# Performance work log

Measured on AMD Instinct MI355X. Metric: run time of the kernel, lower is better.

The kernel has to match this reference:

```python
import jax, jax.numpy as jnp
import numpy as np

N_QUBITS = 4  # matches init n_qubits; depth = 1


def _apply_rx(state, angles, wire):
    # state: (B, 2**N) complex64; angles: (B,) real. RX(theta) = [[c, -is],[-is, c]], c=cos(t/2), s=sin(t/2)
    B = state.shape[0]
    left = 2 ** wire
    st = state.reshape(B, left, 2, -1)
    half = angles * 0.5
    c = jnp.cos(half).astype(jnp.complex64).reshape(B, 1, 1)
    s = ((-1j) * jnp.sin(half).astype(jnp.complex64)).reshape(B, 1, 1)
    s0 = st[:, :, 0, :]
    s1 = st[:, :, 1, :]
    out = jnp.stack([c * s0 + s * s1, s * s0 + c * s1], axis=2)
    return out.reshape(B, -1)


def _apply_cnot(state, ctrl):
    # CNOT on wires [ctrl, ctrl+1]: flip target amplitudes where control bit is 1
    B = state.shape[0]
    left = 2 ** ctrl
    st = state.reshape(B, left, 2, 2, -1)
    st = st.at[:, :, 1, :, :].set(st[:, :, 1, ::-1, :])
    return st.reshape(B, -1)


def _qgate(angles, theta):
    # angles: (B, N_QUBITS) data-encoded RX angles; theta: (N_QUBITS,) trainable RX angles
    # Circuit: RX(data) on each wire -> CNOT chain -> RX(theta) on each wire -> <Z_i> per wire
    B = angles.shape[0]
    state = jnp.zeros((B, 2 ** N_QUBITS), jnp.complex64).at[:, 0].set(1.0 + 0.0j)
    for i in range(N_QUBITS):
        state = _apply_rx(state, angles[:, i], i)
    for i in range(N_QUBITS - 1):
        state = _apply_cnot(state, i)
    for i in range(N_QUBITS):
        state = _apply_rx(state, jnp.broadcast_to(theta[i], (B,)), i)
    probs = jnp.real(state * jnp.conj(state)).reshape((B,) + (2,) * N_QUBITS)
    expz = []
    for i in range(N_QUBITS):
        axes = tuple(a for a in range(1, N_QUBITS + 1) if a != i + 1)
        p = probs.sum(axis=axes)  # (B, 2)
        expz.append(p[:, 0] - p[:, 1])
    return jnp.stack(expz, axis=1)  # (B, N_QUBITS)


def setup_inputs() -> dict:
    key = jax.random.key(0)
    ks = jax.random.split(key, 16)
    T, B, D, H, Q = 256, 512, 128, 128, N_QUBITS

    def w(k, shape, scale=0.05):
        return jax.random.normal(k, shape, jnp.float32) * scale

    inp = {
        'inputs': jax.random.normal(ks[0], (T, B, D), jnp.float32),
        'hx0': jnp.zeros((B, H), jnp.float32),
        'cx0': jnp.zeros((B, H), jnp.float32),
    }
    for j, n in enumerate(['f', 'i', 'g', 'o']):
        inp['W' + n] = w(ks[1 + j], (H, D + H))
        inp['b' + n] = jnp.zeros((H,), jnp.float32)
        inp['W' + n + 'q'] = w(ks[5 + j], (Q, D + H))
        inp['b' + n + 'q'] = jnp.zeros((Q,), jnp.float32)
        inp['th' + n] = jax.random.normal(ks[9 + j], (Q,), jnp.float32)
    inp['Wq'] = w(ks[13], (H, Q))
    inp['bq'] = jnp.zeros((H,), jnp.float32)
    return inp


def reference(inputs, hx0, cx0, Wf, bf, Wfq, bfq, thf, Wi, bi, Wiq, biq, thi,
              Wg, bg, Wgq, bgq, thg, Wo, bo, Woq, boq, tho, Wq, bq):
    def step(carry, x):
        hx, cx = carry
        comb = jnp.concatenate([x, hx], axis=1)  # (B, D+H)

        def lin(W, b):
            return comb @ W.T + b

        def qg(Wl, bl, th):
            return _qgate(lin(Wl, bl), th) @ Wq.T + bq

        f = jax.nn.sigmoid(lin(Wf, bf)) + jax.nn.sigmoid(qg(Wfq, bfq, thf))
        i = jax.nn.sigmoid(lin(Wi, bi)) + jax.nn.sigmoid(qg(Wiq, biq, thi))
        g = jnp.tanh(lin(Wg, bg)) + jnp.tanh(qg(Wgq, bgq, thg))
        o = jax.nn.sigmoid(lin(Wo, bo)) + jax.nn.sigmoid(qg(Woq, boq, tho))
        cx2 = f * cx + i * g
        hx2 = o * jnp.tanh(cx2)
        return (hx2, cx2), hx2

    (hxT, cxT), outs = jax.lax.scan(step, (hx0, cx0), inputs)
    return outs, (hxT, cxT)
```

## Files before the change

### kernel.cpp

```cpp
#include <hip/hip_runtime.h>
#include <cmath>

#define TT 256
#define BB 512
#define DD 128
#define HH 128
#define NCOL 528
#define KK 256
#define NCPAD 576

__global__ __launch_bounds__(256) void pack_weights(
    const float* __restrict__ Wf, const float* __restrict__ bf,
    const float* __restrict__ Wfq, const float* __restrict__ bfq,
    const float* __restrict__ Wi, const float* __restrict__ bi,
    const float* __restrict__ Wiq, const float* __restrict__ biq,
    const float* __restrict__ Wg, const float* __restrict__ bg,
    const float* __restrict__ Wgq, const float* __restrict__ bgq,
    const float* __restrict__ Wo, const float* __restrict__ bo,
    const float* __restrict__ Woq, const float* __restrict__ boq,
    float* __restrict__ Wxp, float* __restrict__ Whr3,
    float* __restrict__ Whql, float* __restrict__ bcat)
{
    int idx = blockIdx.x * blockDim.x + threadIdx.x;
    if (idx < NCOL * KK) {
        int c = idx >> 8, k = idx & 255;
        const float* srcW; int cl;
        if (c < 512) { int g = c >> 7; cl = c & 127;
            srcW = (g == 0) ? Wf : (g == 1) ? Wi : (g == 2) ? Wg : Wo; }
        else { int g = (c - 512) >> 2; cl = (c - 512) & 3;
            srcW = (g == 0) ? Wfq : (g == 1) ? Wiq : (g == 2) ? Wgq : Woq; }
        float v = srcW[(size_t)cl * KK + k];
        if (k < 128) Wxp[(size_t)c * 128 + k] = v;
        else {
            int kk = k - 128;
            if (c < 512) {
                int gate = c >> 7, hcol = c & 127;
                int t = hcol * 4 + (kk >> 5);
                int j = gate * 8 + ((kk >> 2) & 7);
                Whr3[((size_t)j * 512 + t) * 4 + (kk & 3)] = v;
            } else {
                Whql[(size_t)(c - 512) * 128 + kk] = v;
            }
        }
    }
    if (idx < NCPAD) {
        float b = 0.f;
        int c = idx;
        if (c < 512) { int g = c >> 7; int cl = c & 127;
            b = (g == 0) ? bf[cl] : (g == 1) ? bi[cl] : (g == 2) ? bg[cl] : bo[cl]; }
        else if (c < NCOL) { int g = (c - 512) >> 2; int cl = (c - 512) & 3;
            b = (g == 0) ? bfq[cl] : (g == 1) ? biq[cl] : (g == 2) ? bgq[cl] : boq[cl]; }
        bcat[c] = b;
    }
}

#define P1_BM 128
#define P1_BN 64
#define ATP 132
#define BTP 68
__global__ __launch_bounds__(256, 3) void xgemm(
    const float* __restrict__ X, const float* __restrict__ Wxp,
    const float* __restrict__ bcat, float* __restrict__ Zx)
{
    __shared__ float At[64][ATP];
    __shared__ float Bt[64][BTP];
    const int tid = threadIdx.x;
    const int m0 = blockIdx.x * P1_BM;
    const int c0 = blockIdx.y * P1_BN;
    const int tm = tid >> 3;
    const int tn = tid & 7;
    float acc[4][8] = {};

    for (int khf = 0; khf < 2; ++khf) {
        #pragma unroll
        for (int j = 0; j < 8; ++j) {
            int fidx = tid + 256 * j;
            int m = fidx >> 4, k4 = (fidx & 15) * 4;
            float4 v = *(const float4*)(X + (size_t)(m0 + m) * 128 + khf * 64 + k4);
            At[k4 + 0][m] = v.x; At[k4 + 1][m] = v.y; At[k4 + 2][m] = v.z; At[k4 + 3][m] = v.w;
        }
        #pragma unroll
        for (int j = 0; j < 4; ++j) {
            int fidx = tid + 256 * j;
            int c = fidx >> 4, k4 = (fidx & 15) * 4;
            int cg = c0 + c;
            float4 v = make_float4(0.f, 0.f, 0.f, 0.f);
            if (cg < NCOL) v = *(const float4*)(Wxp + (size_t)cg * 128 + khf * 64 + k4);
            Bt[k4 + 0][c] = v.x; Bt[k4 + 1][c] = v.y; Bt[k4 + 2][c] = v.z; Bt[k4 + 3][c] = v.w;
        }
        __syncthreads();
        #pragma unroll 4
        for (int k = 0; k < 64; ++k) {
            float4 a  = *(const float4*)&At[k][tm * 4];
            float4 b0 = *(const float4*)&Bt[k][tn * 8];
            float4 b1 = *(const float4*)&Bt[k][tn * 8 + 4];
            float av[4] = {a.x, a.y, a.z, a.w};
            float bv[8] = {b0.x, b0.y, b0.z, b0.w, b1.x, b1.y, b1.z, b1.w};
            #pragma unroll
            for (int i = 0; i < 4; ++i)
                #pragma unroll
                for (int j = 0; j < 8; ++j)
                    acc[i][j] = fmaf(av[i], bv[j], acc[i][j]);
        }
        __syncthreads();
    }
    int c = c0 + tn * 8;
    if (c < NCOL) {
        float4 ba = *(const float4*)(bcat + c);
        float4 bb = *(const float4*)(bcat + c + 4);
        #pragma unroll
        for (int i = 0; i < 4; ++i) {
            int m = m0 + tm * 4 + i;
            float4 o0, o1;
            o0.x = acc[i][0] + ba.x; o0.y = acc[i][1] + ba.y;
            o0.z = acc[i][2] + ba.z; o0.w = acc[i][3] + ba.w;
            o1.x = acc[i][4] + bb.x; o1.y = acc[i][5] + bb.y;
            o1.z = acc[i][6] + bb.z; o1.w = acc[i][7] + bb.w;
            *(float4*)(Zx + (size_t)m * NCOL + c)     = o0;
            *(float4*)(Zx + (size_t)m * NCOL + c + 4) = o1;
        }
    }
}

__device__ __forceinline__ float sigm(float x) { return 1.0f / (1.0f + __expf(-x)); }
__device__ __forceinline__ float tanh_f(float x) {
    float e = __expf(2.f * x);
    return 1.f - 2.f / (e + 1.f);
}

#define FMA4(acc, Wv, Xv) acc = fmaf((Wv).x, (Xv).x, fmaf((Wv).y, (Xv).y, fmaf((Wv).z, (Xv).z, fmaf((Wv).w, (Xv).w, (acc)))))
#define PIN4(Wv) asm volatile("" : "+v"((Wv).x), "+v"((Wv).y), "+v"((Wv).z), "+v"((Wv).w))

#define DPPRED(v) { \
    v += __int_as_float(__builtin_amdgcn_update_dpp(0, __float_as_int(v), 0xB1, 0xF, 0xF, true)); \
    v += __int_as_float(__builtin_amdgcn_update_dpp(0, __float_as_int(v), 0x4E, 0xF, 0xF, true)); }

__device__ __forceinline__ int hsk(int k) { return k + 8 * (k >> 5); }

__global__ __launch_bounds__(512)
__attribute__((amdgpu_waves_per_eu(2, 2)))
void qlstm_rec(
    const float* __restrict__ Zx,
    const float* __restrict__ Whr3,
    const float* __restrict__ Whql,
    const float* __restrict__ hx0, const float* __restrict__ cx0,
    float* __restrict__ stateH, float* __restrict__ stateC,
    const float* __restrict__ Wq, const float* __restrict__ bq,
    const float* __restrict__ thf, const float* __restrict__ thi,
    const float* __restrict__ thg, const float* __restrict__ tho,
    float* __restrict__ out, int t0, int TC)
{
    __shared__ __align__(16) float hL[2][152];
    __shared__ __align__(16) float cEd[2][20];
    __shared__ __align__(16) float cEc[2][20];

    const int tid  = threadIdx.x;
    const int row0 = blockIdx.x * 2;
    const int ks   = tid & 3;
    const int h    = tid >> 2;

    const float4* Wp3 = (const float4*)Whr3;
    float4 wv[32];
    #pragma unroll
    for (int j = 0; j < 32; ++j) wv[j] = Wp3[j * 512 + tid];
    #pragma unroll
    for (int j = 0; j < 32; ++j) PIN4(wv[j]);

    const bool isCell = (ks < 2);
    const int  r      = ks & 1;
    float4 wqv = make_float4(0.f, 0.f, 0.f, 0.f);
    float bb = 0.f, cxr = 0.f;
    if (isCell) {
        wqv = *(const float4*)(Wq + h * 4);
        bb  = bq[h];
    }
    const bool isQ = (tid & 15) < 4;
    const int qi = tid >> 4;
    const int rq = qi & 1, qc = qi >> 1;
    const int qg = qc >> 2, qw = qc & 3;
    float qcoef = 1.f, qth3 = 0.f;
    float4 qw4[8] = {};
    if (isQ) {
        const float* thp = (qg == 0) ? thf : (qg == 1) ? thi : (qg == 2) ? thg : tho;
        qcoef = (qw < 3) ? cosf(thp[qw]) : 1.f;
        qth3  = thp[3];
        const float4* qp = (const float4*)(Whql + (size_t)qc * 128 + ks * 32);
        #pragma unroll
        for (int j = 0; j < 8; ++j) qw4[j] = qp[j];
    }
    if (isCell) {
        const float* hs = (t0 == 0) ? hx0 : stateH;
        const float* cs = (t0 == 0) ? cx0 : stateC;
        hL[r][hsk(h)] = hs[(size_t)(row0 + r) * HH + h];
        cxr           = cs[(size_t)(row0 + r) * HH + h];
    }
    __syncthreads();

    for (int tc = 0; tc < TC; ++tc) {
        const float* zrow = Zx + ((size_t)tc * BB + row0) * NCOL;
        float zc0 = 0, zc1 = 0, zc2 = 0, zc3 = 0, zqv = 0;
        if (isCell) {
            const float* zp = zrow + (size_t)r * NCOL + h;
            zc0 = zp[0]; zc1 = zp[128]; zc2 = zp[256]; zc3 = zp[384];
        }
        if (isQ) zqv = zrow[(size_t)rq * NCOL + 512 + qc];

        float aF0 = 0, aF1 = 0, aI0 = 0, aI1 = 0, aG0 = 0, aG1 = 0, aO0 = 0, aO1 = 0;
        float qa = 0.f;
        {
            const float4* h0p = (const float4*)&hL[0][40 * ks];
            const float4* h1p = (const float4*)&hL[1][40 * ks];
            #pragma unroll
            for (int k4 = 0; k4 < 8; ++k4) {
                float4 hv0 = h0p[k4];
                float4 hv1 = h1p[k4];
                FMA4(aF0, wv[k4],      hv0);  FMA4(aF1, wv[k4],      hv1);
                FMA4(aI0, wv[8 + k4],  hv0);  FMA4(aI1, wv[8 + k4],  hv1);
                FMA4(aG0, wv[16 + k4], hv0);  FMA4(aG1, wv[16 + k4], hv1);
                FMA4(aO0, wv[24 + k4], hv0);  FMA4(aO1, wv[24 + k4], hv1);
                float4 hq;
                hq.x = rq ? hv1.x : hv0.x; hq.y = rq ? hv1.y : hv0.y;
                hq.z = rq ? hv1.z : hv0.z; hq.w = rq ? hv1.w : hv0.w;
                FMA4(qa, qw4[k4], hq);
            }
        }
        DPPRED(aF0) DPPRED(aF1) DPPRED(aI0) DPPRED(aI1)
        DPPRED(aG0) DPPRED(aG1) DPPRED(aO0) DPPRED(aO1)
        DPPRED(qa)

        if (isQ) {
            float a = zqv + qa;
            float c = __cosf(a);
            float dval = (qw < 3) ? qcoef * c : __cosf(a + qth3);
            if (ks == 0) {
                cEd[rq][qc] = dval;
                cEc[rq][qc] = c;
            }
        }
        __syncthreads();

        if (isCell) {
            float pf = zc0 + (r ? aF1 : aF0);
            float pi = zc1 + (r ? aI1 : aI0);
            float pg = zc2 + (r ? aG1 : aG0);
            float po = zc3 + (r ? aO1 : aO0);
            float qz[4];
            #pragma unroll
            for (int g = 0; g < 4; ++g) {
                float4 dv = *(const float4*)&cEd[r][g * 4];
                float4 cv = *(const float4*)&cEc[r][g * 4];
                float c01  = cv.x * cv.y;
                float c012 = c01 * cv.z;
                qz[g] = fmaf(dv.x, wqv.x,
                        fmaf(dv.y * cv.x, wqv.y,
                        fmaf(dv.z * c01, wqv.z,
                        fmaf(dv.w * c012, wqv.w, bb))));
            }
            float f  = sigm(pf)   + sigm(qz[0]);
            float ii = sigm(pi)   + sigm(qz[1]);
            float gg = tanh_f(pg) + tanh_f(qz[2]);
            float oo = sigm(po)   + sigm(qz[3]);
            float cn = fmaf(f, cxr, ii * gg);
            cxr = cn;
            float hn = oo * tanh_f(cn);
            hL[r][hsk(h)] = hn;
            out[((size_t)(t0 + tc) * BB + row0 + r) * HH + h] = hn;
        }
        __syncthreads();
    }

    if (isCell) {
        float hn = hL[r][hsk(h)];
        stateH[(size_t)(row0 + r) * HH + h] = hn;
        stateC[(size_t)(row0 + r) * HH + h] = cxr;
        if (t0 + TC == TT) {
            size_t base = (size_t)TT * BB * HH;
            out[base + (size_t)(row0 + r) * HH + h]                   = hn;
            out[base + (size_t)BB * HH + (size_t)(row0 + r) * HH + h] = cxr;
        }
    }
}

extern "C" void kernel_launch(void* const* d_in, const int* in_sizes, int n_in,
                              void* d_out, int out_size, void* d_ws, size_t ws_size,
                              hipStream_t stream) {
    const float* X   = (const float*)d_in[0];
    const float* hx0 = (const float*)d_in[1];
    const float* cx0 = (const float*)d_in[2];
    const float* Wf  = (const float*)d_in[3];
    const float* bf  = (const float*)d_in[4];
    const float* Wfq = (const float*)d_in[5];
    const float* bfq = (const float*)d_in[6];
    const float* thf = (const float*)d_in[7];
    const float* Wi  = (const float*)d_in[8];
    const float* bi  = (const float*)d_in[9];
    const float* Wiq = (const float*)d_in[10];
    const float* biq = (const float*)d_in[11];
    const float* thi = (const float*)d_in[12];
    const float* Wg  = (const float*)d_in[13];
    const float* bg  = (const float*)d_in[14];
    const float* Wgq = (const float*)d_in[15];
    const float* bgq = (const float*)d_in[16];
    const float* thg = (const float*)d_in[17];
    const float* Wo  = (const float*)d_in[18];
    const float* bo  = (const float*)d_in[19];
    const float* Woq = (const float*)d_in[20];
    const float* boq = (const float*)d_in[21];
    const float* tho = (const float*)d_in[22];
    const float* Wq  = (const float*)d_in[23];
    const float* bq  = (const float*)d_in[24];

    float* ws = (float*)d_ws;
    float* Wxp    = ws;
    float* Whr3   = Wxp + 528 * 128;
    float* Whql   = Whr3 + 65536;
    float* bcatp  = Whql + 2048;
    float* stateH = bcatp + NCPAD;
    float* stateC = stateH + 512 * 128;
    float* Zxb    = stateC + 512 * 128;

    size_t fixed_bytes = (size_t)(Zxb - ws) * sizeof(float);
    int TC = 256;
    while (TC > 4 && fixed_bytes + (size_t)TC * 512 * NCOL * 4 > ws_size) TC >>= 1;

    pack_weights<<<(NCOL * KK + 255) / 256, 256, 0, stream>>>(
        Wf, bf, Wfq, bfq, Wi, bi, Wiq, biq, Wg, bg, Wgq, bgq, Wo, bo, Woq, boq,
        Wxp, Whr3, Whql, bcatp);

    for (int t0 = 0; t0 < TT; t0 += TC) {
        xgemm<<<dim3(TC * 512 / P1_BM, NCPAD / P1_BN), 256, 0, stream>>>(
            X + (size_t)t0 * BB * DD, Wxp, bcatp, Zxb);
        qlstm_rec<<<256, 512, 0, stream>>>(
            Zxb, Whr3, Whql, hx0, cx0, stateH, stateC, Wq, bq,
            thf, thi, thg, tho, (float*)d_out, t0, TC);
    }
}
```

Baseline: 774.0 us.

## Split recurrent K-reduction across 8 lanes with 1024-thread blocks

```diff
diff --git a/kernel.cpp b/kernel.cpp
--- a/kernel.cpp
+++ b/kernel.cpp
@@ -18,7 +18,7 @@
     const float* __restrict__ Wgq, const float* __restrict__ bgq,
     const float* __restrict__ Wo, const float* __restrict__ bo,
     const float* __restrict__ Woq, const float* __restrict__ boq,
-    float* __restrict__ Wxp, float* __restrict__ Whr3,
+    float* __restrict__ Wxp, float* __restrict__ Whr4,
     float* __restrict__ Whql, float* __restrict__ bcat)
 {
     int idx = blockIdx.x * blockDim.x + threadIdx.x;
@@ -35,9 +35,9 @@
             int kk = k - 128;
             if (c < 512) {
                 int gate = c >> 7, hcol = c & 127;
-                int t = hcol * 4 + (kk >> 5);
-                int j = gate * 8 + ((kk >> 2) & 7);
-                Whr3[((size_t)j * 512 + t) * 4 + (kk & 3)] = v;
+                int t = hcol * 8 + (kk >> 4);
+                int j = gate * 4 + ((kk >> 2) & 3);
+                Whr4[((size_t)j * 1024 + t) * 4 + (kk & 3)] = v;
             } else {
                 Whql[(size_t)(c - 512) * 128 + kk] = v;
             }
@@ -129,19 +129,18 @@
 }
 
 #define FMA4(acc, Wv, Xv) acc = fmaf((Wv).x, (Xv).x, fmaf((Wv).y, (Xv).y, fmaf((Wv).z, (Xv).z, fmaf((Wv).w, (Xv).w, (acc)))))
-#define PIN4(Wv) asm volatile("" : "+v"((Wv).x), "+v"((Wv).y), "+v"((Wv).z), "+v"((Wv).w))
-
+
+#define XOR4RED(v) { \
+    v += __int_as_float(__builtin_amdgcn_ds_swizzle(__float_as_int(v), 0x101F)); }
 #define DPPRED(v) { \
     v += __int_as_float(__builtin_amdgcn_update_dpp(0, __float_as_int(v), 0xB1, 0xF, 0xF, true)); \
     v += __int_as_float(__builtin_amdgcn_update_dpp(0, __float_as_int(v), 0x4E, 0xF, 0xF, true)); }
 
-__device__ __forceinline__ int hsk(int k) { return k + 8 * (k >> 5); }
-
-__global__ __launch_bounds__(512)
-__attribute__((amdgpu_waves_per_eu(2, 2)))
-void qlstm_rec(
+__device__ __forceinline__ int hsk(int k) { return k + 4 * (k >> 4); }
+
+__global__ __launch_bounds__(1024) void qlstm_rec(
     const float* __restrict__ Zx,
-    const float* __restrict__ Whr3,
+    const float* __restrict__ Whr4,
     const float* __restrict__ Whql,
     const float* __restrict__ hx0, const float* __restrict__ cx0,
     float* __restrict__ stateH, float* __restrict__ stateC,
@@ -150,21 +149,26 @@
     const float* __restrict__ thg, const float* __restrict__ tho,
     float* __restrict__ out, int t0, int TC)
 {
-    __shared__ __align__(16) float hL[2][152];
+    __shared__ __align__(16) float hL[2][160];
+    __shared__ __align__(16) float WhqLs[16][160];
     __shared__ __align__(16) float cEd[2][20];
     __shared__ __align__(16) float cEc[2][20];
 
     const int tid  = threadIdx.x;
     const int row0 = blockIdx.x * 2;
-    const int ks   = tid & 3;
-    const int h    = tid >> 2;
-
-    const float4* Wp3 = (const float4*)Whr3;
-    float4 wv[32];
+    const int ks   = tid & 7;
+    const int h    = tid >> 3;
+
+    const float4* Wp4 = (const float4*)Whr4;
+    float4 wv[16];
     #pragma unroll
-    for (int j = 0; j < 32; ++j) wv[j] = Wp3[j * 512 + tid];
+    for (int j = 0; j < 16; ++j) wv[j] = Wp4[j * 1024 + tid];
+
     #pragma unroll
-    for (int j = 0; j < 32; ++j) PIN4(wv[j]);
+    for (int j = 0; j < 2; ++j) {
+        int i = tid + 1024 * j;
+        WhqLs[i >> 7][hsk(i & 127)] = Whql[i];
+    }
 
     const bool isCell = (ks < 2);
     const int  r      = ks & 1;
@@ -174,19 +178,15 @@
         wqv = *(const float4*)(Wq + h * 4);
         bb  = bq[h];
     }
-    const bool isQ = (tid & 15) < 4;
-    const int qi = tid >> 4;
-    const int rq = qi & 1, qc = qi >> 1;
-    const int qg = qc >> 2, qw = qc & 3;
+    const bool isQ = (tid < 256);
+    const int rq  = h & 1;
+    const int qc  = (h >> 1) & 15;
+    const int qg  = qc >> 2, qw = qc & 3;
     float qcoef = 1.f, qth3 = 0.f;
-    float4 qw4[8] = {};
     if (isQ) {
         const float* thp = (qg == 0) ? thf : (qg == 1) ? thi : (qg == 2) ? thg : tho;
         qcoef = (qw < 3) ? cosf(thp[qw]) : 1.f;
         qth3  = thp[3];
-        const float4* qp = (const float4*)(Whql + (size_t)qc * 128 + ks * 32);
-        #pragma unroll
-        for (int j = 0; j < 8; ++j) qw4[j] = qp[j];
     }
     if (isCell) {
         const float* hs = (t0 == 0) ? hx0 : stateH;
@@ -196,34 +196,44 @@
     }
     __syncthreads();
 
+    const float4* h0p = (const float4*)&hL[0][20 * ks];
+    const float4* h1p = (const float4*)&hL[1][20 * ks];
+    const float4* hqp = (const float4*)&hL[rq][20 * ks];
+    const float4* qwp = (const float4*)&WhqLs[qc][20 * ks];
+
+    const float* zbase = Zx + (size_t)row0 * NCOL;
+    float*       outp  = out + (((size_t)t0 * BB) + row0 + r) * HH + h;
+
     for (int tc = 0; tc < TC; ++tc) {
-        const float* zrow = Zx + ((size_t)tc * BB + row0) * NCOL;
         float zc0 = 0, zc1 = 0, zc2 = 0, zc3 = 0, zqv = 0;
         if (isCell) {
-            const float* zp = zrow + (size_t)r * NCOL + h;
+            const float* zp = zbase + (size_t)r * NCOL + h;
             zc0 = zp[0]; zc1 = zp[128]; zc2 = zp[256]; zc3 = zp[384];
         }
-        if (isQ) zqv = zrow[(size_t)rq * NCOL + 512 + qc];
+        if (isQ) zqv = zbase[(size_t)rq * NCOL + 512 + qc];
 
         float aF0 = 0, aF1 = 0, aI0 = 0, aI1 = 0, aG0 = 0, aG1 = 0, aO0 = 0, aO1 = 0;
         float qa = 0.f;
-        {
-            const float4* h0p = (const float4*)&hL[0][40 * ks];
-            const float4* h1p = (const float4*)&hL[1][40 * ks];
+        #pragma unroll
+        for (int k4 = 0; k4 < 4; ++k4) {
+            float4 hv0 = h0p[k4];
+            float4 hv1 = h1p[k4];
+            FMA4(aF0, wv[k4],      hv0);  FMA4(aF1, wv[k4],      hv1);
+            FMA4(aI0, wv[4 + k4],  hv0);  FMA4(aI1, wv[4 + k4],  hv1);
+            FMA4(aG0, wv[8 + k4],  hv0);  FMA4(aG1, wv[8 + k4],  hv1);
+            FMA4(aO0, wv[12 + k4], hv0);  FMA4(aO1, wv[12 + k4], hv1);
+        }
+        if (isQ) {
             #pragma unroll
-            for (int k4 = 0; k4 < 8; ++k4) {
-                float4 hv0 = h0p[k4];
-                float4 hv1 = h1p[k4];
-                FMA4(aF0, wv[k4],      hv0);  FMA4(aF1, wv[k4],      hv1);
-                FMA4(aI0, wv[8 + k4],  hv0);  FMA4(aI1, wv[8 + k4],  hv1);
-                FMA4(aG0, wv[16 + k4], hv0);  FMA4(aG1, wv[16 + k4], hv1);
-                FMA4(aO0, wv[24 + k4], hv0);  FMA4(aO1, wv[24 + k4], hv1);
-                float4 hq;
-                hq.x = rq ? hv1.x : hv0.x; hq.y = rq ? hv1.y : hv0.y;
-                hq.z = rq ? hv1.z : hv0.z; hq.w = rq ? hv1.w : hv0.w;
-                FMA4(qa, qw4[k4], hq);
+            for (int k4 = 0; k4 < 4; ++k4) {
+                float4 wq4 = qwp[k4];
+                float4 hq  = hqp[k4];
+                FMA4(qa, wq4, hq);
             }
         }
+        XOR4RED(aF0) XOR4RED(aF1) XOR4RED(aI0) XOR4RED(aI1)
+        XOR4RED(aG0) XOR4RED(aG1) XOR4RED(aO0) XOR4RED(aO1)
+        XOR4RED(qa)
         DPPRED(aF0) DPPRED(aF1) DPPRED(aI0) DPPRED(aI1)
         DPPRED(aG0) DPPRED(aG1) DPPRED(aO0) DPPRED(aO1)
         DPPRED(qa)
@@ -264,9 +274,11 @@
             cxr = cn;
             float hn = oo * tanh_f(cn);
             hL[r][hsk(h)] = hn;
-            out[((size_t)(t0 + tc) * BB + row0 + r) * HH + h] = hn;
+            *outp = hn;
         }
         __syncthreads();
+        zbase += (size_t)BB * NCOL;
+        outp  += (size_t)BB * HH;
     }
 
     if (isCell) {
@@ -312,8 +324,8 @@
 
     float* ws = (float*)d_ws;
     float* Wxp    = ws;
-    float* Whr3   = Wxp + 528 * 128;
-    float* Whql   = Whr3 + 65536;
+    float* Whr4   = Wxp + 528 * 128;
+    float* Whql   = Whr4 + 65536;
     float* bcatp  = Whql + 2048;
     float* stateH = bcatp + NCPAD;
     float* stateC = stateH + 512 * 128;
@@ -325,13 +337,13 @@
 
     pack_weights<<<(NCOL * KK + 255) / 256, 256, 0, stream>>>(
         Wf, bf, Wfq, bfq, Wi, bi, Wiq, biq, Wg, bg, Wgq, bgq, Wo, bo, Woq, boq,
-        Wxp, Whr3, Whql, bcatp);
+        Wxp, Whr4, Whql, bcatp);
 
     for (int t0 = 0; t0 < TT; t0 += TC) {
         xgemm<<<dim3(TC * 512 / P1_BM, NCPAD / P1_BN), 256, 0, stream>>>(
             X + (size_t)t0 * BB * DD, Wxp, bcatp, Zxb);
-        qlstm_rec<<<256, 512, 0, stream>>>(
-            Zxb, Whr3, Whql, hx0, cx0, stateH, stateC, Wq, bq,
+        qlstm_rec<<<256, 1024, 0, stream>>>(
+            Zxb, Whr4, Whql, hx0, cx0, stateH, stateC, Wq, bq,
             thf, thi, thg, tho, (float*)d_out, t0, TC);
     }
 }
```

New measurement: 1.702 ms. +119.9%, slower.

## Move recurrent h·W matmul to bf16 MFMA with hi/lo split, 16 rows per block

Applied to the files above, without the earlier changes.

```diff
diff --git a/kernel.cpp b/kernel.cpp
--- a/kernel.cpp
+++ b/kernel.cpp
@@ -8,6 +8,21 @@
 #define NCOL 528
 #define KK 256
 #define NCPAD 576
+#define RWG 16
+#define NWGR (BB/RWG)
+#define NTILE 33
+
+typedef __attribute__((ext_vector_type(8))) short short8v;
+typedef __attribute__((ext_vector_type(4))) float f32x4;
+
+__device__ __forceinline__ unsigned short f2bf(float x) {
+    unsigned u = __float_as_uint(x);
+    u += 0x7FFFu + ((u >> 16) & 1u);
+    return (unsigned short)(u >> 16);
+}
+__device__ __forceinline__ float bf2f(unsigned short b) {
+    return __uint_as_float(((unsigned)b) << 16);
+}
 
 __global__ __launch_bounds__(256) void pack_weights(
     const float* __restrict__ Wf, const float* __restrict__ bf,
@@ -18,34 +33,33 @@
     const float* __restrict__ Wgq, const float* __restrict__ bgq,
     const float* __restrict__ Wo, const float* __restrict__ bo,
     const float* __restrict__ Woq, const float* __restrict__ boq,
-    float* __restrict__ Wxp, float* __restrict__ Whr3,
-    float* __restrict__ Whql, float* __restrict__ bcat)
+    float* __restrict__ Wxp, unsigned short* __restrict__ Whb,
+    float* __restrict__ bcat)
 {
     int idx = blockIdx.x * blockDim.x + threadIdx.x;
-    if (idx < NCOL * KK) {
-        int c = idx >> 8, k = idx & 255;
+    auto wval = [&](int c, int k) -> float {
         const float* srcW; int cl;
         if (c < 512) { int g = c >> 7; cl = c & 127;
             srcW = (g == 0) ? Wf : (g == 1) ? Wi : (g == 2) ? Wg : Wo; }
         else { int g = (c - 512) >> 2; cl = (c - 512) & 3;
             srcW = (g == 0) ? Wfq : (g == 1) ? Wiq : (g == 2) ? Wgq : Woq; }
-        float v = srcW[(size_t)cl * KK + k];
-        if (k < 128) Wxp[(size_t)c * 128 + k] = v;
-        else {
-            int kk = k - 128;
-            if (c < 512) {
-                int gate = c >> 7, hcol = c & 127;
-                int t = hcol * 4 + (kk >> 5);
-                int j = gate * 8 + ((kk >> 2) & 7);
-                Whr3[((size_t)j * 512 + t) * 4 + (kk & 3)] = v;
-            } else {
-                Whql[(size_t)(c - 512) * 128 + kk] = v;
-            }
-        }
+        return srcW[(size_t)cl * KK + k];
+    };
+    if (idx < NTILE * 4 * 2 * 512) {
+        int e = idx & 7, l = (idx >> 3) & 63, hl = (idx >> 9) & 1;
+        int kf = (idx >> 10) & 3, t = idx >> 12;
+        int c = t * 16 + (l & 15);
+        int k = kf * 32 + ((l >> 4) << 3) + e;
+        float v = wval(c, 128 + k);
+        unsigned short hi = f2bf(v);
+        Whb[idx] = hl ? f2bf(v - bf2f(hi)) : hi;
+    }
+    if (idx < NCOL * 128) {
+        int c = idx >> 7, k = idx & 127;
+        Wxp[(size_t)c * 128 + k] = wval(c, k);
     }
     if (idx < NCPAD) {
-        float b = 0.f;
-        int c = idx;
+        float b = 0.f; int c = idx;
         if (c < 512) { int g = c >> 7; int cl = c & 127;
             b = (g == 0) ? bf[cl] : (g == 1) ? bi[cl] : (g == 2) ? bg[cl] : bo[cl]; }
         else if (c < NCOL) { int g = (c - 512) >> 2; int cl = (c - 512) & 3;
@@ -127,22 +141,16 @@
     float e = __expf(2.f * x);
     return 1.f - 2.f / (e + 1.f);
 }
-
-#define FMA4(acc, Wv, Xv) acc = fmaf((Wv).x, (Xv).x, fmaf((Wv).y, (Xv).y, fmaf((Wv).z, (Xv).z, fmaf((Wv).w, (Xv).w, (acc)))))
-#define PIN4(Wv) asm volatile("" : "+v"((Wv).x), "+v"((Wv).y), "+v"((Wv).z), "+v"((Wv).w))
-
-#define DPPRED(v) { \
-    v += __int_as_float(__builtin_amdgcn_update_dpp(0, __float_as_int(v), 0xB1, 0xF, 0xF, true)); \
-    v += __int_as_float(__builtin_amdgcn_update_dpp(0, __float_as_int(v), 0x4E, 0xF, 0xF, true)); }
-
-__device__ __forceinline__ int hsk(int k) { return k + 8 * (k >> 5); }
+__device__ __forceinline__ int scol(int c) { return c + 4 * (c >> 5); }
+__device__ __forceinline__ int wsk(int h)  { return h + ((h >> 5) & 3); }
+
+#define MFMA(a, b, c) __builtin_amdgcn_mfma_f32_16x16x32_bf16((a), (b), (c), 0, 0, 0)
 
 __global__ __launch_bounds__(512)
 __attribute__((amdgpu_waves_per_eu(2, 2)))
 void qlstm_rec(
     const float* __restrict__ Zx,
-    const float* __restrict__ Whr3,
-    const float* __restrict__ Whql,
+    const unsigned short* __restrict__ Whb,
     const float* __restrict__ hx0, const float* __restrict__ cx0,
     float* __restrict__ stateH, float* __restrict__ stateC,
     const float* __restrict__ Wq, const float* __restrict__ bq,
@@ -150,133 +158,188 @@
     const float* __restrict__ thg, const float* __restrict__ tho,
     float* __restrict__ out, int t0, int TC)
 {
-    __shared__ __align__(16) float hL[2][152];
-    __shared__ __align__(16) float cEd[2][20];
-    __shared__ __align__(16) float cEc[2][20];
+    __shared__ __align__(16) float S[16][600];
+    __shared__ __align__(16) unsigned short hHi[16][136];
+    __shared__ __align__(16) unsigned short hLo[16][136];
+    __shared__ __align__(16) float cEd[16][16];
+    __shared__ __align__(16) float cEc[16][16];
+    __shared__ float WqT[4][160];
+    __shared__ float bqS[160];
 
     const int tid  = threadIdx.x;
-    const int row0 = blockIdx.x * 2;
-    const int ks   = tid & 3;
-    const int h    = tid >> 2;
-
-    const float4* Wp3 = (const float4*)Whr3;
-    float4 wv[32];
+    const int wid  = tid >> 6, lane = tid & 63;
+    const int row0g = blockIdx.x * RWG;
+
+    short8v Bhi[5][4], Blo[5][4];
     #pragma unroll
-    for (int j = 0; j < 32; ++j) wv[j] = Wp3[j * 512 + tid];
-    #pragma unroll
-    for (int j = 0; j < 32; ++j) PIN4(wv[j]);
-
-    const bool isCell = (ks < 2);
-    const int  r      = ks & 1;
-    float4 wqv = make_float4(0.f, 0.f, 0.f, 0.f);
-    float bb = 0.f, cxr = 0.f;
-    if (isCell) {
-        wqv = *(const float4*)(Wq + h * 4);
-        bb  = bq[h];
-    }
-    const bool isQ = (tid & 15) < 4;
-    const int qi = tid >> 4;
-    const int rq = qi & 1, qc = qi >> 1;
-    const int qg = qc >> 2, qw = qc & 3;
+    for (int i = 0; i < 5; ++i) {
+        int t = (i < 4) ? (wid * 4 + i) : 32;
+        #pragma unroll
+        for (int kf = 0; kf < 4; ++kf) {
+            size_t base = (size_t)((t * 4 + kf) * 2) * 512 + (size_t)lane * 8;
+            Bhi[i][kf] = *(const short8v*)(Whb + base);
+            Blo[i][kf] = *(const short8v*)(Whb + base + 512);
+        }
+    }
+
+    if (tid < 128) {
+        int s = wsk(tid);
+        WqT[0][s] = Wq[tid * 4 + 0]; WqT[1][s] = Wq[tid * 4 + 1];
+        WqT[2][s] = Wq[tid * 4 + 2]; WqT[3][s] = Wq[tid * 4 + 3];
+        bqS[s] = bq[tid];
+    }
+
+    const int qc = lane & 15, qg = qc >> 2, qw = qc & 3;
     float qcoef = 1.f, qth3 = 0.f;
-    float4 qw4[8] = {};
-    if (isQ) {
+    if (wid == 7) {
         const float* thp = (qg == 0) ? thf : (qg == 1) ? thi : (qg == 2) ? thg : tho;
         qcoef = (qw < 3) ? cosf(thp[qw]) : 1.f;
         qth3  = thp[3];
-        const float4* qp = (const float4*)(Whql + (size_t)qc * 128 + ks * 32);
-        #pragma unroll
-        for (int j = 0; j < 8; ++j) qw4[j] = qp[j];
-    }
-    if (isCell) {
+    }
+
+    const int crow = tid >> 5;
+    const int hb   = (tid & 31) * 4;
+
+    float4 cx4, hlast;
+    {
         const float* hs = (t0 == 0) ? hx0 : stateH;
         const float* cs = (t0 == 0) ? cx0 : stateC;
-        hL[r][hsk(h)] = hs[(size_t)(row0 + r) * HH + h];
-        cxr           = cs[(size_t)(row0 + r) * HH + h];
+        float4 h4 = *(const float4*)(hs + (size_t)(row0g + crow) * HH + hb);
+        cx4 = *(const float4*)(cs + (size_t)(row0g + crow) * HH + hb);
+        hlast = h4;
+        #pragma unroll
+        for (int j = 0; j < 4; ++j) {
+            float hv = (&h4.x)[j];
+            unsigned short hi = f2bf(hv);
+            hHi[crow][hb + j] = hi;
+            hLo[crow][hb + j] = f2bf(hv - bf2f(hi));
+        }
     }
     __syncthreads();
 
+    const float* zstep = Zx + (size_t)row0g * NCOL;
+    float* outp = out + ((size_t)t0 * BB + row0g + crow) * HH + hb;
+
+    float4 zc0 = *(const float4*)(zstep + (size_t)crow * NCOL + 0 * 128 + hb);
+    float4 zc1 = *(const float4*)(zstep + (size_t)crow * NCOL + 1 * 128 + hb);
+    float4 zc2 = *(const float4*)(zstep + (size_t)crow * NCOL + 2 * 128 + hb);
+    float4 zc3 = *(const float4*)(zstep + (size_t)crow * NCOL + 3 * 128 + hb);
+    float zq0 = 0, zq1 = 0, zq2 = 0, zq3 = 0;
+    if (wid == 7) {
+        int rb4 = (lane >> 4) * 4;
+        zq0 = zstep[(size_t)(rb4 + 0) * NCOL + 512 + qc];
+        zq1 = zstep[(size_t)(rb4 + 1) * NCOL + 512 + qc];
+        zq2 = zstep[(size_t)(rb4 + 2) * NCOL + 512 + qc];
+        zq3 = zstep[(size_t)(rb4 + 3) * NCOL + 512 + qc];
+    }
+
     for (int tc = 0; tc < TC; ++tc) {
-        const float* zrow = Zx + ((size_t)tc * BB + row0) * NCOL;
-        float zc0 = 0, zc1 = 0, zc2 = 0, zc3 = 0, zqv = 0;
-        if (isCell) {
-            const float* zp = zrow + (size_t)r * NCOL + h;
-            zc0 = zp[0]; zc1 = zp[128]; zc2 = zp[256]; zc3 = zp[384];
-        }
-        if (isQ) zqv = zrow[(size_t)rq * NCOL + 512 + qc];
-
-        float aF0 = 0, aF1 = 0, aI0 = 0, aI1 = 0, aG0 = 0, aG1 = 0, aO0 = 0, aO1 = 0;
-        float qa = 0.f;
+        const size_t noff = (tc + 1 < TC) ? (size_t)BB * NCOL : 0;
+
+        const int arow = lane & 15, kb = (lane >> 4) * 8;
+        f32x4 C0 = {0,0,0,0}, C1 = {0,0,0,0}, C2 = {0,0,0,0}, C3 = {0,0,0,0}, C4 = {0,0,0,0};
+        #pragma unroll
+        for (int kf = 0; kf < 4; ++kf) {
+            short8v Ahi = *(const short8v*)&hHi[arow][kf * 32 + kb];
+            short8v Alo = *(const short8v*)&hLo[arow][kf * 32 + kb];
+            C0 = MFMA(Ahi, Bhi[0][kf], C0); C0 = MFMA(Alo, Bhi[0][kf], C0); C0 = MFMA(Ahi, Blo[0][kf], C0);
+            C1 = MFMA(Ahi, Bhi[1][kf], C1); C1 = MFMA(Alo, Bhi[1][kf], C1); C1 = MFMA(Ahi, Blo[1][kf], C1);
+            C2 = MFMA(Ahi, Bhi[2][kf], C2); C2 = MFMA(Alo, Bhi[2][kf], C2); C2 = MFMA(Ahi, Blo[2][kf], C2);
+            C3 = MFMA(Ahi, Bhi[3][kf], C3); C3 = MFMA(Alo, Bhi[3][kf], C3); C3 = MFMA(Ahi, Blo[3][kf], C3);
+            if (wid == 7) {
+                C4 = MFMA(Ahi, Bhi[4][kf], C4); C4 = MFMA(Alo, Bhi[4][kf], C4); C4 = MFMA(Ahi, Blo[4][kf], C4);
+            }
+        }
         {
-            const float4* h0p = (const float4*)&hL[0][40 * ks];
-            const float4* h1p = (const float4*)&hL[1][40 * ks];
-            #pragma unroll
-            for (int k4 = 0; k4 < 8; ++k4) {
-                float4 hv0 = h0p[k4];
-                float4 hv1 = h1p[k4];
-                FMA4(aF0, wv[k4],      hv0);  FMA4(aF1, wv[k4],      hv1);
-                FMA4(aI0, wv[8 + k4],  hv0);  FMA4(aI1, wv[8 + k4],  hv1);
-                FMA4(aG0, wv[16 + k4], hv0);  FMA4(aG1, wv[16 + k4], hv1);
-                FMA4(aO0, wv[24 + k4], hv0);  FMA4(aO1, wv[24 + k4], hv1);
-                float4 hq;
-                hq.x = rq ? hv1.x : hv0.x; hq.y = rq ? hv1.y : hv0.y;
-                hq.z = rq ? hv1.z : hv0.z; hq.w = rq ? hv1.w : hv0.w;
-                FMA4(qa, qw4[k4], hq);
-            }
-        }
-        DPPRED(aF0) DPPRED(aF1) DPPRED(aI0) DPPRED(aI1)
-        DPPRED(aG0) DPPRED(aG1) DPPRED(aO0) DPPRED(aO1)
-        DPPRED(qa)
-
-        if (isQ) {
-            float a = zqv + qa;
-            float c = __cosf(a);
-            float dval = (qw < 3) ? qcoef * c : __cosf(a + qth3);
-            if (ks == 0) {
-                cEd[rq][qc] = dval;
-                cEc[rq][qc] = c;
-            }
+            const int cl = lane & 15, rb = (lane >> 4) * 4;
+            #define SWRITE(Ci, ii) { int col = (wid * 4 + (ii)) * 16 + cl; int sc = scol(col); \
+                S[rb + 0][sc] = (Ci)[0]; S[rb + 1][sc] = (Ci)[1]; \
+                S[rb + 2][sc] = (Ci)[2]; S[rb + 3][sc] = (Ci)[3]; }
+            SWRITE(C0, 0) SWRITE(C1, 1) SWRITE(C2, 2) SWRITE(C3, 3)
+            #undef SWRITE
+        }
+        if (wid == 7) {
+            int rb4 = (lane >> 4) * 4;
+            float a0 = C4[0] + zq0, a1 = C4[1] + zq1, a2 = C4[2] + zq2, a3 = C4[3] + zq3;
+            float c0_ = __cosf(a0), c1_ = __cosf(a1), c2_ = __cosf(a2), c3_ = __cosf(a3);
+            float d0 = (qw < 3) ? qcoef * c0_ : __cosf(a0 + qth3);
+            float d1 = (qw < 3) ? qcoef * c1_ : __cosf(a1 + qth3);
+            float d2 = (qw < 3) ? qcoef * c2_ : __cosf(a2 + qth3);
+            float d3 = (qw < 3) ? qcoef * c3_ : __cosf(a3 + qth3);
+            cEd[rb4 + 0][qc] = d0; cEc[rb4 + 0][qc] = c0_;
+            cEd[rb4 + 1][qc] = d1; cEc[rb4 + 1][qc] = c1_;
+            cEd[rb4 + 2][qc] = d2; cEc[rb4 + 2][qc] = c2_;
+            cEd[rb4 + 3][qc] = d3; cEc[rb4 + 3][qc] = c3_;
+            zq0 = zstep[noff + (size_t)(rb4 + 0) * NCOL + 512 + qc];
+            zq1 = zstep[noff + (size_t)(rb4 + 1) * NCOL + 512 + qc];
+            zq2 = zstep[noff + (size_t)(rb4 + 2) * NCOL + 512 + qc];
+            zq3 = zstep[noff + (size_t)(rb4 + 3) * NCOL + 512 + qc];
         }
         __syncthreads();
 
-        if (isCell) {
-            float pf = zc0 + (r ? aF1 : aF0);
-            float pi = zc1 + (r ? aI1 : aI0);
-            float pg = zc2 + (r ? aG1 : aG0);
-            float po = zc3 + (r ? aO1 : aO0);
-            float qz[4];
+        {
+            float4 sv0 = *(const float4*)&S[crow][scol(0 * 128 + hb)];
+            float4 sv1 = *(const float4*)&S[crow][scol(1 * 128 + hb)];
+            float4 sv2 = *(const float4*)&S[crow][scol(2 * 128 + hb)];
+            float4 sv3 = *(const float4*)&S[crow][scol(3 * 128 + hb)];
+            float4 pre0, pre1, pre2, pre3;
+            pre0.x = zc0.x + sv0.x; pre0.y = zc0.y + sv0.y; pre0.z = zc0.z + sv0.z; pre0.w = zc0.w + sv0.w;
+            pre1.x = zc1.x + sv1.x; pre1.y = zc1.y + sv1.y; pre1.z = zc1.z + sv1.z; pre1.w = zc1.w + sv1.w;
+            pre2.x = zc2.x + sv2.x; pre2.y = zc2.y + sv2.y; pre2.z = zc2.z + sv2.z; pre2.w = zc2.w + sv2.w;
+            pre3.x = zc3.x + sv3.x; pre3.y = zc3.y + sv3.y; pre3.z = zc3.z + sv3.z; pre3.w = zc3.w + sv3.w;
+            zc0 = *(const float4*)(zstep + noff + (size_t)crow * NCOL + 0 * 128 + hb);
+            zc1 = *(const float4*)(zstep + noff + (size_t)crow * NCOL + 1 * 128 + hb);
+            zc2 = *(const float4*)(zstep + noff + (size_t)crow * NCOL + 2 * 128 + hb);
+            zc3 = *(const float4*)(zstep + noff + (size_t)crow * NCOL + 3 * 128 + hb);
+            float E[4][4];
             #pragma unroll
             for (int g = 0; g < 4; ++g) {
-                float4 dv = *(const float4*)&cEd[r][g * 4];
-                float4 cv = *(const float4*)&cEc[r][g * 4];
-                float c01  = cv.x * cv.y;
-                float c012 = c01 * cv.z;
-                qz[g] = fmaf(dv.x, wqv.x,
-                        fmaf(dv.y * cv.x, wqv.y,
-                        fmaf(dv.z * c01, wqv.z,
-                        fmaf(dv.w * c012, wqv.w, bb))));
+                float4 dv = *(const float4*)&cEd[crow][g * 4];
+                float4 cv = *(const float4*)&cEc[crow][g * 4];
+                float c01 = cv.x * cv.y;
+                E[g][0] = dv.x;
+                E[g][1] = dv.y * cv.x;
+                E[g][2] = dv.z * c01;
+                E[g][3] = dv.w * (c01 * cv.z);
             }
-            float f  = sigm(pf)   + sigm(qz[0]);
-            float ii = sigm(pi)   + sigm(qz[1]);
-            float gg = tanh_f(pg) + tanh_f(qz[2]);
-            float oo = sigm(po)   + sigm(qz[3]);
-            float cn = fmaf(f, cxr, ii * gg);
-            cxr = cn;
-            float hn = oo * tanh_f(cn);
-            hL[r][hsk(h)] = hn;
-            out[((size_t)(t0 + tc) * BB + row0 + r) * HH + h] = hn;
+            float4 hres;
+            #pragma unroll
+            for (int j = 0; j < 4; ++j) {
+                int s = wsk(hb + j);
+                float wq0 = WqT[0][s], wq1 = WqT[1][s], wq2 = WqT[2][s], wq3 = WqT[3][s];
+                float bb = bqS[s];
+                float qzf = fmaf(E[0][0], wq0, fmaf(E[0][1], wq1, fmaf(E[0][2], wq2, fmaf(E[0][3], wq3, bb))));
+                float qzi = fmaf(E[1][0], wq0, fmaf(E[1][1], wq1, fmaf(E[1][2], wq2, fmaf(E[1][3], wq3, bb))));
+                float qzg = fmaf(E[2][0], wq0, fmaf(E[2][1], wq1, fmaf(E[2][2], wq2, fmaf(E[2][3], wq3, bb))));
+                float qzo = fmaf(E[3][0], wq0, fmaf(E[3][1], wq1, fmaf(E[3][2], wq2, fmaf(E[3][3], wq3, bb))));
+                float f  = sigm((&pre0.x)[j])   + sigm(qzf);
+                float ii = sigm((&pre1.x)[j])   + sigm(qzi);
+                float gg = tanh_f((&pre2.x)[j]) + tanh_f(qzg);
+                float oo = sigm((&pre3.x)[j])   + sigm(qzo);
+                float cn = fmaf(f, (&cx4.x)[j], ii * gg);
+                (&cx4.x)[j] = cn;
+                float hn = oo * tanh_f(cn);
+                (&hres.x)[j] = hn;
+                unsigned short hi = f2bf(hn);
+                hHi[crow][hb + j] = hi;
+                hLo[crow][hb + j] = f2bf(hn - bf2f(hi));
+            }
+            *(float4*)outp = hres;
+            hlast = hres;
         }
         __syncthreads();
-    }
-
-    if (isCell) {
-        float hn = hL[r][hsk(h)];
-        stateH[(size_t)(row0 + r) * HH + h] = hn;
-        stateC[(size_t)(row0 + r) * HH + h] = cxr;
+        zstep += (size_t)BB * NCOL;
+        outp  += (size_t)BB * HH;
+    }
+
+    {
+        size_t off = (size_t)(row0g + crow) * HH + hb;
+        *(float4*)(stateH + off) = hlast;
+        *(float4*)(stateC + off) = cx4;
         if (t0 + TC == TT) {
             size_t base = (size_t)TT * BB * HH;
-            out[base + (size_t)(row0 + r) * HH + h]                   = hn;
-            out[base + (size_t)BB * HH + (size_t)(row0 + r) * HH + h] = cxr;
+            *(float4*)(out + base + off) = hlast;
+            *(float4*)(out + base + (size_t)BB * HH + off) = cx4;
         }
     }
 }
@@ -312,26 +375,26 @@
 
     float* ws = (float*)d_ws;
     float* Wxp    = ws;
-    float* Whr3   = Wxp + 528 * 128;
-    float* Whql   = Whr3 + 65536;
-    float* bcatp  = Whql + 2048;
-    float* stateH = bcatp + NCPAD;
-    float* stateC = stateH + 512 * 128;
-    float* Zxb    = stateC + 512 * 128;
+    float* bcatp  = Wxp + 67584;
+    float* stateH = bcatp + 576;
+    float* stateC = stateH + 65536;
+    unsigned short* Whb = (unsigned short*)(stateC + 65536);
+    float* Zxb    = stateC + 65536 + 67584;
 
     size_t fixed_bytes = (size_t)(Zxb - ws) * sizeof(float);
     int TC = 256;
     while (TC > 4 && fixed_bytes + (size_t)TC * 512 * NCOL * 4 > ws_size) TC >>= 1;
 
-    pack_weights<<<(NCOL * KK + 255) / 256, 256, 0, stream>>>(
+    int packN = NTILE * 4 * 2 * 512;
+    pack_weights<<<(packN + 255) / 256, 256, 0, stream>>>(
         Wf, bf, Wfq, bfq, Wi, bi, Wiq, biq, Wg, bg, Wgq, bgq, Wo, bo, Woq, boq,
-        Wxp, Whr3, Whql, bcatp);
+        Wxp, Whb, bcatp);
 
     for (int t0 = 0; t0 < TT; t0 += TC) {
         xgemm<<<dim3(TC * 512 / P1_BM, NCPAD / P1_BN), 256, 0, stream>>>(
             X + (size_t)t0 * BB * DD, Wxp, bcatp, Zxb);
-        qlstm_rec<<<256, 512, 0, stream>>>(
-            Zxb, Whr3, Whql, hx0, cx0, stateH, stateC, Wq, bq,
+        qlstm_rec<<<NWGR, 512, 0, stream>>>(
+            Zxb, Whb, hx0, cx0, stateH, stateC, Wq, bq,
             thf, thi, thg, tho, (float*)d_out, t0, TC);
     }
 }
```

Measured after the change: 1.293 ms. +67.1%, slower.
